# Performance work log

Hardware: AMD Instinct MI355X
Metric: run time of the kernel (lower is better)

Reference implementation:

```python
import jax, jax.numpy as jnp
import numpy as np

D, H, W = 160, 192, 160


def _grid_sample_3d(vol, grid):
    """torch F.grid_sample (3D, bilinear/trilinear, padding='zeros', align_corners=False).
    vol: [B,C,D,H,W]; grid: [B,Do,Ho,Wo,3], last dim ordered (x,y,z) in [-1,1]."""
    B, C, Dv, Hv, Wv = vol.shape
    x, y, z = grid[..., 0], grid[..., 1], grid[..., 2]
    # align_corners=False unnormalization
    ix = ((x + 1.0) * Wv - 1.0) * 0.5
    iy = ((y + 1.0) * Hv - 1.0) * 0.5
    iz = ((z + 1.0) * Dv - 1.0) * 0.5
    fx, fy, fz = jnp.floor(ix), jnp.floor(iy), jnp.floor(iz)
    wx, wy, wz = ix - fx, iy - fy, iz - fz
    ix0, iy0, iz0 = fx.astype(jnp.int32), fy.astype(jnp.int32), fz.astype(jnp.int32)
    vol_flat = vol.reshape(B, C, Dv * Hv * Wv)
    out_sp = x.shape[1:]  # (Do, Ho, Wo)

    def gather(zi, yi, xi):
        inb = ((zi >= 0) & (zi < Dv) & (yi >= 0) & (yi < Hv) & (xi >= 0) & (xi < Wv))
        lin = ((jnp.clip(zi, 0, Dv - 1) * Hv + jnp.clip(yi, 0, Hv - 1)) * Wv
               + jnp.clip(xi, 0, Wv - 1)).reshape(B, -1)
        vals = jax.vmap(lambda v, i: v[:, i])(vol_flat, lin)  # [B,C,N]
        return vals.reshape((B, C) + out_sp) * inb[:, None].astype(vol.dtype)

    out = jnp.zeros((B, C) + tuple(out_sp), vol.dtype)
    # fixed 8-corner trilinear accumulation
    for dz, wz_ in ((0, 1.0 - wz), (1, wz)):
        for dy, wy_ in ((0, 1.0 - wy), (1, wy)):
            for dx, wx_ in ((0, 1.0 - wx), (1, wx)):
                w = (wz_ * wy_ * wx_)[:, None]  # [B,1,Do,Ho,Wo]
                out = out + w * gather(iz0 + dz, iy0 + dy, ix0 + dx)
    return out


def _voxel_grid():
    gd, gh, gw = jnp.meshgrid(jnp.arange(D, dtype=jnp.float32),
                              jnp.arange(H, dtype=jnp.float32),
                              jnp.arange(W, dtype=jnp.float32), indexing='ij')
    return jnp.stack([gd, gh, gw])[None]  # [1,3,D,H,W], channels (d,h,w)


def _to_xyz(t):
    # [B,3,D,H,W] channels (d,h,w) -> [B,D,H,W,3] channels (x,y,z)
    return jnp.moveaxis(t, 1, -1)[..., ::-1]


def setup_inputs() -> dict:
    key = jax.random.key(0)
    k1, k2, k3 = jax.random.split(key, 3)
    src = jax.random.normal(k1, (1, 1, D, H, W), dtype=jnp.float32)
    flow1 = jax.random.normal(k2, (1, 3, D, H, W), dtype=jnp.float32)
    flow2 = jax.random.normal(k3, (1, 3, D, H, W), dtype=jnp.float32)
    range_flow = jnp.float32(0.4)
    return {"src": src, "flow1": flow1, "flow2": flow2, "range_flow": range_flow}


def reference(src, flow1, flow2, range_flow):
    grid = _voxel_grid()  # voxel-coordinate identity grid
    # NOTE: grid2 is intentionally NOT normalized to [-1,1] (faithful to source quirk)
    grid2 = _to_xyz(grid + flow2 * range_flow)
    flow1_warped = _grid_sample_3d(flow1, grid2)
    out_flow = flow1_warped + flow2
    denom = jnp.array([D - 1, H - 1, W - 1], jnp.float32).reshape(1, 3, 1, 1, 1)
    new_locs_total = 2.0 * ((grid + out_flow * range_flow) / denom - 0.5)
    deform_2_img = _grid_sample_3d(src, _to_xyz(new_locs_total))
    return deform_2_img, out_flow
```

## Files before the change

### kernel.cpp

```cpp
#include <hip/hip_runtime.h>

constexpr int Dv = 160, Hv = 192, Wv = 160;
constexpr int NN = Dv * Hv * Wv;

__device__ __forceinline__ float tri_sample_1c(const float* __restrict__ v,
                                               float x, float y, float z) {
  float ix = ((x + 1.0f) * (float)Wv - 1.0f) * 0.5f;
  float iy = ((y + 1.0f) * (float)Hv - 1.0f) * 0.5f;
  float iz = ((z + 1.0f) * (float)Dv - 1.0f) * 0.5f;
  float fx = floorf(ix), fy = floorf(iy), fz = floorf(iz);
  float wx = ix - fx, wy = iy - fy, wz = iz - fz;
  int x0 = (int)fx, y0 = (int)fy, z0 = (int)fz;
  float acc = 0.0f;
#pragma unroll
  for (int c = 0; c < 8; ++c) {
    const int dz = (c >> 2) & 1, dy = (c >> 1) & 1, dx = c & 1;
    int zi = z0 + dz, yi = y0 + dy, xi = x0 + dx;
    if ((unsigned)zi < (unsigned)Dv && (unsigned)yi < (unsigned)Hv &&
        (unsigned)xi < (unsigned)Wv) {
      float wgt = (dz ? wz : 1.0f - wz) * (dy ? wy : 1.0f - wy) *
                  (dx ? wx : 1.0f - wx);
      acc += wgt * v[(zi * Hv + yi) * Wv + xi];
    }
  }
  return acc;
}

__device__ __forceinline__ void tri_sample_3c(const float* __restrict__ v,
                                              float x, float y, float z,
                                              float& o0, float& o1, float& o2) {
  o0 = 0.0f; o1 = 0.0f; o2 = 0.0f;
  float ix = ((x + 1.0f) * (float)Wv - 1.0f) * 0.5f;
  float iy = ((y + 1.0f) * (float)Hv - 1.0f) * 0.5f;
  float iz = ((z + 1.0f) * (float)Dv - 1.0f) * 0.5f;
  float fx = floorf(ix), fy = floorf(iy), fz = floorf(iz);
  float wx = ix - fx, wy = iy - fy, wz = iz - fz;
  int x0 = (int)fx, y0 = (int)fy, z0 = (int)fz;
  if (x0 < -1 || x0 >= Wv || y0 < -1 || y0 >= Hv || z0 < -1 || z0 >= Dv)
    return;
#pragma unroll
  for (int c = 0; c < 8; ++c) {
    const int dz = (c >> 2) & 1, dy = (c >> 1) & 1, dx = c & 1;
    int zi = z0 + dz, yi = y0 + dy, xi = x0 + dx;
    if ((unsigned)zi < (unsigned)Dv && (unsigned)yi < (unsigned)Hv &&
        (unsigned)xi < (unsigned)Wv) {
      float wgt = (dz ? wz : 1.0f - wz) * (dy ? wy : 1.0f - wy) *
                  (dx ? wx : 1.0f - wx);
      int lin = (zi * Hv + yi) * Wv + xi;
      o0 += wgt * v[lin];
      o1 += wgt * v[NN + lin];
      o2 += wgt * v[2 * NN + lin];
    }
  }
}

__global__ __launch_bounds__(256)
void st_fused_kernel(const float* __restrict__ src,
                     const float* __restrict__ flow1,
                     const float* __restrict__ flow2,
                     const float* __restrict__ rfp,
                     float* __restrict__ out) {
  int idx = blockIdx.x * blockDim.x + threadIdx.x;
  if (idx >= NN) return;
  const float rf = rfp[0];

  int w = idx % Wv;
  int t = idx / Wv;
  int h = t % Hv;
  int d = t / Hv;

  float f2_0 = flow2[idx];
  float f2_1 = flow2[NN + idx];
  float f2_2 = flow2[2 * NN + idx];

  float gx = (float)w + rf * f2_2;
  float gy = (float)h + rf * f2_1;
  float gz = (float)d + rf * f2_0;

  float w0, w1, w2;
  tri_sample_3c(flow1, gx, gy, gz, w0, w1, w2);

  float of0 = w0 + f2_0;
  float of1 = w1 + f2_1;
  float of2 = w2 + f2_2;

  out[NN + idx] = of0;
  out[2 * NN + idx] = of1;
  out[3 * NN + idx] = of2;

  float nl0 = 2.0f * (((float)d + of0 * rf) / (float)(Dv - 1) - 0.5f);
  float nl1 = 2.0f * (((float)h + of1 * rf) / (float)(Hv - 1) - 0.5f);
  float nl2 = 2.0f * (((float)w + of2 * rf) / (float)(Wv - 1) - 0.5f);

  float img = tri_sample_1c(src, nl2, nl1, nl0);
  out[idx] = img;
}

extern "C" void kernel_launch(void* const* d_in, const int* in_sizes, int n_in,
                              void* d_out, int out_size, void* d_ws, size_t ws_size,
                              hipStream_t stream) {
  const float* src   = (const float*)d_in[0];
  const float* flow1 = (const float*)d_in[1];
  const float* flow2 = (const float*)d_in[2];
  const float* rfp   = (const float*)d_in[3];
  float* out = (float*)d_out;

  const int threads = 256;
  const int blocks = (NN + threads - 1) / threads;
  hipLaunchKernelGGL(st_fused_kernel, dim3(blocks), dim3(threads), 0, stream,
                     src, flow1, flow2, rfp, out);
}
```

Baseline: 197.7 us.

## Process four voxels per thread with float4 I/O and branchless trilinear gather

Each thread now handles four consecutive voxels, loading flow2 and storing all outputs with float4 vector accesses. The second trilinear sample becomes branchless: out-of-bounds corners get zero weight and clamped indices, so all eight loads are issued without divergence. This aims to cut memory instruction count and divergence. In exchange it uses more registers per thread and launches a quarter as many threads, which may reduce the latency hiding available for the random gathers.

New measurement: 199.4 us. About the same (+0.9%).

```diff
diff --git a/kernel.cpp b/kernel.cpp
--- a/kernel.cpp
+++ b/kernel.cpp
@@ -2,42 +2,52 @@
 
 constexpr int Dv = 160, Hv = 192, Wv = 160;
 constexpr int NN = Dv * Hv * Wv;
+constexpr int N4 = NN / 4;
 
-__device__ __forceinline__ float tri_sample_1c(const float* __restrict__ v,
-                                               float x, float y, float z) {
-  float ix = ((x + 1.0f) * (float)Wv - 1.0f) * 0.5f;
-  float iy = ((y + 1.0f) * (float)Hv - 1.0f) * 0.5f;
-  float iz = ((z + 1.0f) * (float)Dv - 1.0f) * 0.5f;
+__device__ __forceinline__ float tri1(const float* __restrict__ v,
+                                      float ix, float iy, float iz) {
   float fx = floorf(ix), fy = floorf(iy), fz = floorf(iz);
   float wx = ix - fx, wy = iy - fy, wz = iz - fz;
   int x0 = (int)fx, y0 = (int)fy, z0 = (int)fz;
-  float acc = 0.0f;
-#pragma unroll
-  for (int c = 0; c < 8; ++c) {
-    const int dz = (c >> 2) & 1, dy = (c >> 1) & 1, dx = c & 1;
-    int zi = z0 + dz, yi = y0 + dy, xi = x0 + dx;
-    if ((unsigned)zi < (unsigned)Dv && (unsigned)yi < (unsigned)Hv &&
-        (unsigned)xi < (unsigned)Wv) {
-      float wgt = (dz ? wz : 1.0f - wz) * (dy ? wy : 1.0f - wy) *
-                  (dx ? wx : 1.0f - wx);
-      acc += wgt * v[(zi * Hv + yi) * Wv + xi];
-    }
-  }
-  return acc;
+  int x1 = x0 + 1, y1 = y0 + 1, z1 = z0 + 1;
+  float wx0 = ((unsigned)x0 < (unsigned)Wv) ? (1.0f - wx) : 0.0f;
+  float wx1 = ((unsigned)x1 < (unsigned)Wv) ? wx : 0.0f;
+  float wy0 = ((unsigned)y0 < (unsigned)Hv) ? (1.0f - wy) : 0.0f;
+  float wy1 = ((unsigned)y1 < (unsigned)Hv) ? wy : 0.0f;
+  float wz0 = ((unsigned)z0 < (unsigned)Dv) ? (1.0f - wz) : 0.0f;
+  float wz1 = ((unsigned)z1 < (unsigned)Dv) ? wz : 0.0f;
+  int xa0 = min(max(x0, 0), Wv - 1), xa1 = min(max(x1, 0), Wv - 1);
+  int ya0 = min(max(y0, 0), Hv - 1), ya1 = min(max(y1, 0), Hv - 1);
+  int za0 = min(max(z0, 0), Dv - 1), za1 = min(max(z1, 0), Dv - 1);
+  int r00 = (za0 * Hv + ya0) * Wv;
+  int r01 = (za0 * Hv + ya1) * Wv;
+  int r10 = (za1 * Hv + ya0) * Wv;
+  int r11 = (za1 * Hv + ya1) * Wv;
+  float v000 = v[r00 + xa0], v001 = v[r00 + xa1];
+  float v010 = v[r01 + xa0], v011 = v[r01 + xa1];
+  float v100 = v[r10 + xa0], v101 = v[r10 + xa1];
+  float v110 = v[r11 + xa0], v111 = v[r11 + xa1];
+  float c00 = v000 * wx0 + v001 * wx1;
+  float c01 = v010 * wx0 + v011 * wx1;
+  float c10 = v100 * wx0 + v101 * wx1;
+  float c11 = v110 * wx0 + v111 * wx1;
+  float c0 = c00 * wy0 + c01 * wy1;
+  float c1 = c10 * wy0 + c11 * wy1;
+  return c0 * wz0 + c1 * wz1;
 }
 
-__device__ __forceinline__ void tri_sample_3c(const float* __restrict__ v,
-                                              float x, float y, float z,
-                                              float& o0, float& o1, float& o2) {
+__device__ __forceinline__ void tri3_rare(const float* __restrict__ v,
+                                          float gx, float gy, float gz,
+                                          float& o0, float& o1, float& o2) {
   o0 = 0.0f; o1 = 0.0f; o2 = 0.0f;
-  float ix = ((x + 1.0f) * (float)Wv - 1.0f) * 0.5f;
-  float iy = ((y + 1.0f) * (float)Hv - 1.0f) * 0.5f;
-  float iz = ((z + 1.0f) * (float)Dv - 1.0f) * 0.5f;
+  float ix = ((gx + 1.0f) * (float)Wv - 1.0f) * 0.5f;
+  float iy = ((gy + 1.0f) * (float)Hv - 1.0f) * 0.5f;
+  float iz = ((gz + 1.0f) * (float)Dv - 1.0f) * 0.5f;
   float fx = floorf(ix), fy = floorf(iy), fz = floorf(iz);
-  float wx = ix - fx, wy = iy - fy, wz = iz - fz;
   int x0 = (int)fx, y0 = (int)fy, z0 = (int)fz;
   if (x0 < -1 || x0 >= Wv || y0 < -1 || y0 >= Hv || z0 < -1 || z0 >= Dv)
     return;
+  float wx = ix - fx, wy = iy - fy, wz = iz - fz;
 #pragma unroll
   for (int c = 0; c < 8; ++c) {
     const int dz = (c >> 2) & 1, dy = (c >> 1) & 1, dx = c & 1;
@@ -55,45 +65,59 @@
 }
 
 __global__ __launch_bounds__(256)
-void st_fused_kernel(const float* __restrict__ src,
-                     const float* __restrict__ flow1,
-                     const float* __restrict__ flow2,
-                     const float* __restrict__ rfp,
-                     float* __restrict__ out) {
-  int idx = blockIdx.x * blockDim.x + threadIdx.x;
-  if (idx >= NN) return;
+void st_fused4_kernel(const float* __restrict__ src,
+                      const float* __restrict__ flow1,
+                      const float* __restrict__ flow2,
+                      const float* __restrict__ rfp,
+                      float* __restrict__ out) {
+  int t4 = blockIdx.x * blockDim.x + threadIdx.x;
+  if (t4 >= N4) return;
   const float rf = rfp[0];
 
-  int w = idx % Wv;
-  int t = idx / Wv;
-  int h = t % Hv;
-  int d = t / Hv;
+  int idx = t4 << 2;
+  int w0 = idx % Wv;
+  int tt = idx / Wv;
+  int h = tt % Hv;
+  int d = tt / Hv;
 
-  float f2_0 = flow2[idx];
-  float f2_1 = flow2[NN + idx];
-  float f2_2 = flow2[2 * NN + idx];
+  float4 f2d = *(const float4*)(flow2 + idx);
+  float4 f2h = *(const float4*)(flow2 + NN + idx);
+  float4 f2w = *(const float4*)(flow2 + 2 * NN + idx);
 
-  float gx = (float)w + rf * f2_2;
-  float gy = (float)h + rf * f2_1;
-  float gz = (float)d + rf * f2_0;
+  float f20[4] = {f2d.x, f2d.y, f2d.z, f2d.w};
+  float f21[4] = {f2h.x, f2h.y, f2h.z, f2h.w};
+  float f22[4] = {f2w.x, f2w.y, f2w.z, f2w.w};
 
-  float w0, w1, w2;
-  tri_sample_3c(flow1, gx, gy, gz, w0, w1, w2);
+  float of0[4], of1[4], of2[4], img[4];
 
-  float of0 = w0 + f2_0;
-  float of1 = w1 + f2_1;
-  float of2 = w2 + f2_2;
+#pragma unroll
+  for (int j = 0; j < 4; ++j) {
+    float wj = (float)(w0 + j);
+    float gx = wj + rf * f22[j];
+    float gy = (float)h + rf * f21[j];
+    float gz = (float)d + rf * f20[j];
 
-  out[NN + idx] = of0;
-  out[2 * NN + idx] = of1;
-  out[3 * NN + idx] = of2;
+    float a0, a1, a2;
+    tri3_rare(flow1, gx, gy, gz, a0, a1, a2);
 
-  float nl0 = 2.0f * (((float)d + of0 * rf) / (float)(Dv - 1) - 0.5f);
-  float nl1 = 2.0f * (((float)h + of1 * rf) / (float)(Hv - 1) - 0.5f);
-  float nl2 = 2.0f * (((float)w + of2 * rf) / (float)(Wv - 1) - 0.5f);
+    of0[j] = a0 + f20[j];
+    of1[j] = a1 + f21[j];
+    of2[j] = a2 + f22[j];
 
-  float img = tri_sample_1c(src, nl2, nl1, nl0);
-  out[idx] = img;
+    float nld = 2.0f * (((float)d + of0[j] * rf) / (float)(Dv - 1) - 0.5f);
+    float nlh = 2.0f * (((float)h + of1[j] * rf) / (float)(Hv - 1) - 0.5f);
+    float nlw = 2.0f * ((wj + of2[j] * rf) / (float)(Wv - 1) - 0.5f);
+
+    float ix = ((nlw + 1.0f) * (float)Wv - 1.0f) * 0.5f;
+    float iy = ((nlh + 1.0f) * (float)Hv - 1.0f) * 0.5f;
+    float iz = ((nld + 1.0f) * (float)Dv - 1.0f) * 0.5f;
+    img[j] = tri1(src, ix, iy, iz);
+  }
+
+  *(float4*)(out + idx)          = make_float4(img[0], img[1], img[2], img[3]);
+  *(float4*)(out + NN + idx)     = make_float4(of0[0], of0[1], of0[2], of0[3]);
+  *(float4*)(out + 2 * NN + idx) = make_float4(of1[0], of1[1], of1[2], of1[3]);
+  *(float4*)(out + 3 * NN + idx) = make_float4(of2[0], of2[1], of2[2], of2[3]);
 }
 
 extern "C" void kernel_launch(void* const* d_in, const int* in_sizes, int n_in,
@@ -106,7 +130,7 @@
   float* out = (float*)d_out;
 
   const int threads = 256;
-  const int blocks = (NN + threads - 1) / threads;
-  hipLaunchKernelGGL(st_fused_kernel, dim3(blocks), dim3(threads), 0, stream,
+  const int blocks = (N4 + threads - 1) / threads;
+  hipLaunchKernelGGL(st_fused4_kernel, dim3(blocks), dim3(threads), 0, stream,
                      src, flow1, flow2, rfp, out);
 }
```
